# Kernel tuning notes

Measured on AMD Instinct MI355X. Metric: run time of the kernel, lower is better.

Reference implementation:

```python
import jax, jax.numpy as jnp
import numpy as np

D_MODEL = 1024
NHEAD = 16
D_HEAD = D_MODEL // NHEAD


def setup_inputs() -> dict:
    key = jax.random.key(0)
    ks = jax.random.split(key, 11)
    B, S = 4, 1024
    s = 1.0 / np.sqrt(D_MODEL)
    inp = {
        'q_in': jax.random.normal(ks[0], (B, S, D_MODEL), jnp.float32),
        'k_in': jax.random.normal(ks[1], (B, S, D_MODEL), jnp.float32),
        'v_in': jax.random.normal(ks[2], (B, S, D_MODEL), jnp.float32),
        'Wq': jax.random.normal(ks[3], (D_MODEL, D_MODEL), jnp.float32) * s,
        'bq': jnp.zeros((D_MODEL,), jnp.float32),
        'Wk': jax.random.normal(ks[4], (D_MODEL, D_MODEL), jnp.float32) * s,
        'bk': jnp.zeros((D_MODEL,), jnp.float32),
        'Wv': jax.random.normal(ks[5], (D_MODEL, D_MODEL), jnp.float32) * s,
        'bv': jnp.zeros((D_MODEL,), jnp.float32),
        'Wo': jax.random.normal(ks[6], (D_MODEL, D_MODEL), jnp.float32) * s,
        'bo': jnp.zeros((D_MODEL,), jnp.float32),
    }
    return inp


def reference(q_in, k_in, v_in, Wq, bq, Wk, bk, Wv, bv, Wo, bo):
    B, Sq, _ = q_in.shape
    Sk = k_in.shape[1]
    # Linear projections (torch Linear: x @ W.T + b; here W stored as [in, out])
    Q = q_in @ Wq + bq
    K = k_in @ Wk + bk
    V = v_in @ Wv + bv
    # [B, H, S, Dh]
    Qh = Q.reshape(B, Sq, NHEAD, D_HEAD).transpose(0, 2, 1, 3)
    Kh = K.reshape(B, Sk, NHEAD, D_HEAD).transpose(0, 2, 1, 3)
    Vh = V.reshape(B, Sk, NHEAD, D_HEAD).transpose(0, 2, 1, 3)
    scores = jnp.einsum('bhqd,bhkd->bhqk', Qh, Kh) / jnp.sqrt(jnp.float32(D_HEAD))
    attn_weights = jax.nn.softmax(scores, axis=-1)
    attn = jnp.einsum('bhqk,bhkd->bhqd', attn_weights, Vh)
    attn = attn.transpose(0, 2, 1, 3).reshape(B, Sq, D_MODEL)
    out = attn @ Wo + bo
    return out
```

## Files before the change

kernel.cpp:

```cpp
#include <hip/hip_runtime.h>
#include <hip/hip_bf16.h>
#include <cstdint>
#include <cstddef>

typedef __bf16 bf16_t;
typedef __bf16 bf16x8 __attribute__((ext_vector_type(8)));
typedef __bf16 bf16x4 __attribute__((ext_vector_type(4)));
typedef float f32x4 __attribute__((ext_vector_type(4)));

#define DM 1024
#define NHEAD 16
#define DHEAD 64

#define QSCALE 0.18033688011112042f
#define PSHIFT 4.0f
#define RS 72

__device__ __forceinline__ void gload_lds16(const void* g, void* l) {
    __builtin_amdgcn_global_load_lds(
        (const __attribute__((address_space(1))) void*)g,
        (__attribute__((address_space(3))) void*)l,
        16, 0, 0);
}

__device__ __forceinline__ uint4 cvt8(float4 lo, float4 hi) {
    union { bf16_t b[8]; uint4 u; } o;
    o.b[0] = (bf16_t)lo.x; o.b[1] = (bf16_t)lo.y; o.b[2] = (bf16_t)lo.z; o.b[3] = (bf16_t)lo.w;
    o.b[4] = (bf16_t)hi.x; o.b[5] = (bf16_t)hi.y; o.b[6] = (bf16_t)hi.z; o.b[7] = (bf16_t)hi.w;
    return o.u;
}

__global__ void prep(
    const float* __restrict__ q_in, const float* __restrict__ k_in, const float* __restrict__ v_in,
    bf16_t* __restrict__ Xq, bf16_t* __restrict__ Xk, bf16_t* __restrict__ Xv,
    const float* __restrict__ w0, const float* __restrict__ w1,
    const float* __restrict__ w2, const float* __restrict__ w3,
    bf16_t* __restrict__ t0, bf16_t* __restrict__ t1,
    bf16_t* __restrict__ t2, bf16_t* __restrict__ t3)
{
    __shared__ float tile[64][65];
    int id = blockIdx.x;
    if (id < 6144) {
        int plane = id >> 11;
        int blk = id & 2047;
        const float* x = plane == 0 ? q_in : plane == 1 ? k_in : v_in;
        bf16_t* y      = plane == 0 ? Xq   : plane == 1 ? Xk   : Xv;
        int i = (blk * 256 + threadIdx.x) * 8;
        float4 lo = *(const float4*)&x[i];
        float4 hi = *(const float4*)&x[i + 4];
        *(uint4*)&y[i] = cvt8(lo, hi);
    } else {
        int t = id - 6144;
        int zi = t >> 8;
        int blk = t & 255;
        const float* w = zi == 0 ? w0 : zi == 1 ? w1 : zi == 2 ? w2 : w3;
        bf16_t* wt     = zi == 0 ? t0 : zi == 1 ? t1 : zi == 2 ? t2 : t3;
        int bx = (blk & 15) * 64;
        int by = (blk >> 4) * 64;
        int tx = threadIdx.x & 63, ty = threadIdx.x >> 6;
        for (int j = 0; j < 64; j += 4)
            tile[ty + j][tx] = w[(size_t)(by + ty + j) * DM + bx + tx];
        __syncthreads();
        int nl = threadIdx.x >> 3;
        int kl = (threadIdx.x & 7) * 8;
        for (int j = 0; j < 64; j += 32) {
            int n = nl + j;
            union { bf16_t b[8]; uint4 u; } o;
            for (int i = 0; i < 8; i++)
                o.b[i] = (bf16_t)tile[kl + i][n];
            *(uint4*)&wt[(size_t)(bx + n) * DM + by + kl] = o.u;
        }
    }
}

template <int MODE>
__device__ __forceinline__ void gemm_body(
    const bf16_t* __restrict__ A, const bf16_t* __restrict__ Bt,
    const float* __restrict__ bias, float scale,
    float* __restrict__ Cf, bf16_t* __restrict__ Cb,
    int r0, int c0, bf16_t* AsP, bf16_t* BsP)
{
    const int K = 1024;
    int tid  = threadIdx.x;
    int wave = tid >> 6;
    int lane = tid & 63;
    int quad = lane >> 4;
    int ln   = lane & 15;
    int wr   = wave >> 1;
    int wc   = wave & 1;

    f32x4 acc[4][4];
    for (int rb = 0; rb < 4; rb++)
        for (int cb = 0; cb < 4; cb++)
            acc[rb][cb] = (f32x4){0.f, 0.f, 0.f, 0.f};

    int sr = tid >> 2;
    int sk = (tid & 3) * 8;

    const bf16_t* gA0 = &A[(size_t)(r0 + sr) * K + sk];
    const bf16_t* gA1 = gA0 + (size_t)64 * K;
    const bf16_t* gB0 = &Bt[(size_t)(c0 + sr) * K + sk];
    const bf16_t* gB1 = gB0 + (size_t)64 * K;
    char* lA = (char*)AsP + wave * 1024;
    char* lB = (char*)BsP + wave * 1024;

    gload_lds16(gA0, lA);
    gload_lds16(gA1, lA + 4096);
    gload_lds16(gB0, lB);
    gload_lds16(gB1, lB + 4096);
    __syncthreads();

    int cur = 0;
    for (int k0 = 0; k0 < K; k0 += 32) {
        int nxt = cur ^ 1;
        if (k0 + 32 < K) {
            int off = nxt * 8192;
            gload_lds16(gA0 + k0 + 32, lA + off);
            gload_lds16(gA1 + k0 + 32, lA + off + 4096);
            gload_lds16(gB0 + k0 + 32, lB + off);
            gload_lds16(gB1 + k0 + 32, lB + off + 4096);
        }
        const bf16_t* Ab = AsP + cur * 4096;
        const bf16_t* Bb = BsP + cur * 4096;

        bf16x8 af[4], bfv[4];
        for (int rb = 0; rb < 4; rb++)
            af[rb] = *(const bf16x8*)&Ab[(wr * 64 + rb * 16 + ln) * 32 + quad * 8];
        for (int cb = 0; cb < 4; cb++)
            bfv[cb] = *(const bf16x8*)&Bb[(wc * 64 + cb * 16 + ln) * 32 + quad * 8];
        for (int rb = 0; rb < 4; rb++)
            for (int cb = 0; cb < 4; cb++)
                acc[rb][cb] = __builtin_amdgcn_mfma_f32_16x16x32_bf16(af[rb], bfv[cb], acc[rb][cb], 0, 0, 0);

        __syncthreads();
        cur = nxt;
    }

    for (int rb = 0; rb < 4; rb++) {
        for (int cb = 0; cb < 4; cb++) {
            int C = c0 + wc * 64 + cb * 16 + ln;
            for (int r = 0; r < 4; r++) {
                int R = r0 + wr * 64 + rb * 16 + quad * 4 + r;
                float v = acc[rb][cb][r];
                if (MODE == 0) {
                    Cf[(size_t)R * DM + C] = v + bias[C];
                } else if (MODE == 1) {
                    int b = R >> 10, s = R & 1023;
                    int h = C >> 6,  d = C & 63;
                    Cb[(((size_t)b * NHEAD + h) * 1024 + s) * DHEAD + d] =
                        (bf16_t)((v + bias[C]) * scale);
                } else {
                    Cb[((size_t)(C >> 10) * 1024 + R) * 1024 + (C & 1023)] =
                        (bf16_t)(v + bias[R]);
                }
            }
        }
    }
}

__global__ __launch_bounds__(256) void gemm_qkv(
    const bf16_t* __restrict__ Xq, const bf16_t* __restrict__ Xk, const bf16_t* __restrict__ Xv,
    const bf16_t* __restrict__ Wtq, const bf16_t* __restrict__ Wtk, const bf16_t* __restrict__ Wtv,
    const float* __restrict__ bq, const float* __restrict__ bk, const float* __restrict__ bv,
    bf16_t* __restrict__ Qd, bf16_t* __restrict__ Kd, bf16_t* __restrict__ Vt)
{
    __shared__ __align__(16) bf16_t As[2 * 128 * 32];
    __shared__ __align__(16) bf16_t Bs[2 * 128 * 32];
    int z = blockIdx.z;
    if (z == 0) {
        gemm_body<1>(Xq, Wtq, bq, QSCALE, nullptr, Qd,
                     blockIdx.x * 128, blockIdx.y * 128, As, Bs);
    } else if (z == 1) {
        gemm_body<1>(Xk, Wtk, bk, 1.0f, nullptr, Kd,
                     blockIdx.x * 128, blockIdx.y * 128, As, Bs);
    } else {
        gemm_body<2>(Wtv, Xv, bv, 1.0f, nullptr, Vt,
                     blockIdx.y * 128, blockIdx.x * 128, As, Bs);
    }
}

__global__ __launch_bounds__(256) void gemm_out(
    const bf16_t* __restrict__ At, const bf16_t* __restrict__ Wto,
    const float* __restrict__ bo, float* __restrict__ out)
{
    const int K = 1024;
    __shared__ __align__(16) bf16_t As[2 * 64 * 32];
    __shared__ __align__(16) bf16_t Bs[2 * 128 * 32];

    int tid  = threadIdx.x;
    int wave = tid >> 6;
    int lane = tid & 63;
    int quad = lane >> 4;
    int ln   = lane & 15;

    int r0 = blockIdx.x * 64;
    int c0 = blockIdx.y * 128;

    f32x4 acc[4][2];
    for (int rb = 0; rb < 4; rb++)
        for (int cb = 0; cb < 2; cb++)
            acc[rb][cb] = (f32x4){0.f, 0.f, 0.f, 0.f};

    int sr = tid >> 2;
    int sk = (tid & 3) * 8;

    const bf16_t* gA0 = At  + (size_t)(r0 + sr) * K + sk;
    const bf16_t* gB0 = Wto + (size_t)(c0 + sr) * K + sk;
    const bf16_t* gB1 = gB0 + (size_t)64 * K;
    char* lA = (char*)As + wave * 1024;
    char* lB = (char*)Bs + wave * 1024;

    gload_lds16(gA0, lA);
    gload_lds16(gB0, lB);
    gload_lds16(gB1, lB + 4096);
    __syncthreads();

    int cur = 0;
    for (int k0 = 0; k0 < K; k0 += 32) {
        int nxt = cur ^ 1;
        if (k0 + 32 < K) {
            gload_lds16(gA0 + k0 + 32, lA + nxt * 4096);
            gload_lds16(gB0 + k0 + 32, lB + nxt * 8192);
            gload_lds16(gB1 + k0 + 32, lB + nxt * 8192 + 4096);
        }
        const bf16_t* Ab = As + cur * 2048;
        const bf16_t* Bb = Bs + cur * 4096;

        bf16x8 af[4], bfv[2];
        for (int rb = 0; rb < 4; rb++)
            af[rb] = *(const bf16x8*)&Ab[(rb * 16 + ln) * 32 + quad * 8];
        for (int cb = 0; cb < 2; cb++)
            bfv[cb] = *(const bf16x8*)&Bb[(wave * 32 + cb * 16 + ln) * 32 + quad * 8];
        for (int rb = 0; rb < 4; rb++)
            for (int cb = 0; cb < 2; cb++)
                acc[rb][cb] = __builtin_amdgcn_mfma_f32_16x16x32_bf16(af[rb], bfv[cb], acc[rb][cb], 0, 0, 0);

        __syncthreads();
        cur = nxt;
    }

    for (int rb = 0; rb < 4; rb++) {
        for (int cb = 0; cb < 2; cb++) {
            int C = c0 + wave * 32 + cb * 16 + ln;
            float bn = bo[C];
            for (int r = 0; r < 4; r++) {
                int R = r0 + rb * 16 + quad * 4 + r;
                out[(size_t)R * DM + C] = acc[rb][cb][r] + bn;
            }
        }
    }
}

__global__ __launch_bounds__(256) void attn6(
    const bf16_t* __restrict__ Q,
    const bf16_t* __restrict__ K,
    const bf16_t* __restrict__ Vt,
    bf16_t* __restrict__ O)
{
    __shared__ __align__(16) bf16_t Ks[64 * RS];
    __shared__ __align__(16) bf16_t Vs[64 * RS];
    __shared__ __align__(16) bf16_t Ps[4][32 * RS];

    int tid  = threadIdx.x;
    int wave = tid >> 6;
    int lane = tid & 63;
    int quad = lane >> 4;
    int ln   = lane & 15;

    int bh = blockIdx.x;
    int q0w = blockIdx.y * 128 + wave * 32;

    const bf16_t* Qb = Q  + (size_t)bh * 65536;
    const bf16_t* Kb = K  + (size_t)bh * 65536;
    const bf16_t* Vb = Vt + (size_t)bh * 65536;

    int srow = tid >> 3;
    int scol = (tid & 7) * 8;
    const bf16_t* gK0 = Kb + (size_t)srow * 64 + scol;
    const bf16_t* gK1 = gK0 + 32 * 64;
    const bf16_t* gV0 = Vb + (size_t)srow * 1024 + scol;
    const bf16_t* gV1 = gV0 + 32 * 1024;

    bf16x8 aq0[2], aq1[2];
    for (int h = 0; h < 2; h++) {
        aq0[h] = *(const bf16x8*)&Qb[(size_t)(q0w + h * 16 + ln) * 64 + quad * 8];
        aq1[h] = *(const bf16x8*)&Qb[(size_t)(q0w + h * 16 + ln) * 64 + 32 + quad * 8];
    }

    uint4 rK0 = *(const uint4*)gK0;
    uint4 rK1 = *(const uint4*)gK1;
    uint4 rV0 = *(const uint4*)gV0;
    uint4 rV1 = *(const uint4*)gV1;

    float l_lane[2] = {0.f, 0.f};
    f32x4 o_acc[2][4];
    for (int h = 0; h < 2; h++)
        for (int cb = 0; cb < 4; cb++)
            o_acc[h][cb] = (f32x4){0.f, 0.f, 0.f, 0.f};

    bf16_t* Pw = Ps[wave];

    for (int kt = 0; kt < 16; kt++) {
        __syncthreads();
        *(uint4*)&Ks[srow * RS + scol]        = rK0;
        *(uint4*)&Ks[(32 + srow) * RS + scol] = rK1;
        *(uint4*)&Vs[srow * RS + scol]        = rV0;
        *(uint4*)&Vs[(32 + srow) * RS + scol] = rV1;
        __syncthreads();

        if (kt < 15) {
            gK0 += 4096; gK1 += 4096; gV0 += 64; gV1 += 64;
            rK0 = *(const uint4*)gK0;
            rK1 = *(const uint4*)gK1;
            rV0 = *(const uint4*)gV0;
            rV1 = *(const uint4*)gV1;
        }

        f32x4 sc[4][2];
        for (int kb = 0; kb < 4; kb++) {
            bf16x8 kf0 = *(const bf16x8*)&Ks[(kb * 16 + ln) * RS + quad * 8];
            bf16x8 kf1 = *(const bf16x8*)&Ks[(kb * 16 + ln) * RS + 32 + quad * 8];
            for (int h = 0; h < 2; h++) {
                f32x4 a = (f32x4){0.f, 0.f, 0.f, 0.f};
                a = __builtin_amdgcn_mfma_f32_16x16x32_bf16(kf0, aq0[h], a, 0, 0, 0);
                a = __builtin_amdgcn_mfma_f32_16x16x32_bf16(kf1, aq1[h], a, 0, 0, 0);
                sc[kb][h] = a;
            }
        }

        for (int kb = 0; kb < 4; kb++) {
            for (int h = 0; h < 2; h++) {
                float p0 = __builtin_amdgcn_exp2f(sc[kb][h][0] - PSHIFT);
                float p1 = __builtin_amdgcn_exp2f(sc[kb][h][1] - PSHIFT);
                float p2 = __builtin_amdgcn_exp2f(sc[kb][h][2] - PSHIFT);
                float p3 = __builtin_amdgcn_exp2f(sc[kb][h][3] - PSHIFT);
                l_lane[h] += (p0 + p1) + (p2 + p3);
                bf16x4 pk = (bf16x4){(bf16_t)p0, (bf16_t)p1, (bf16_t)p2, (bf16_t)p3};
                *(bf16x4*)&Pw[(h * 16 + ln) * RS + kb * 16 + quad * 4] = pk;
            }
        }

        for (int kc = 0; kc < 2; kc++) {
            bf16x8 ap0 = *(const bf16x8*)&Pw[ln * RS + kc * 32 + quad * 8];
            bf16x8 ap1 = *(const bf16x8*)&Pw[(16 + ln) * RS + kc * 32 + quad * 8];
            for (int cb = 0; cb < 4; cb++) {
                bf16x8 vf = *(const bf16x8*)&Vs[(cb * 16 + ln) * RS + kc * 32 + quad * 8];
                o_acc[0][cb] = __builtin_amdgcn_mfma_f32_16x16x32_bf16(ap0, vf, o_acc[0][cb], 0, 0, 0);
                o_acc[1][cb] = __builtin_amdgcn_mfma_f32_16x16x32_bf16(ap1, vf, o_acc[1][cb], 0, 0, 0);
            }
        }
    }

    int b = bh >> 4, hd = bh & 15;
    for (int h = 0; h < 2; h++) {
        float l = l_lane[h];
        l += __shfl_xor(l, 16);
        l += __shfl_xor(l, 32);
        float invq[4];
        for (int r = 0; r < 4; r++)
            invq[r] = 1.f / __shfl(l, quad * 4 + r);
        for (int cb = 0; cb < 4; cb++) {
            for (int r = 0; r < 4; r++) {
                int q = q0w + h * 16 + quad * 4 + r;
                int d = cb * 16 + ln;
                O[((size_t)b * 1024 + q) * DM + hd * 64 + d] = (bf16_t)(o_acc[h][cb][r] * invq[r]);
            }
        }
    }
}

extern "C" void kernel_launch(void* const* d_in, const int* in_sizes, int n_in,
                              void* d_out, int out_size, void* d_ws, size_t ws_size,
                              hipStream_t stream) {
    const float* q_in = (const float*)d_in[0];
    const float* k_in = (const float*)d_in[1];
    const float* v_in = (const float*)d_in[2];
    const float* Wq   = (const float*)d_in[3];
    const float* bq   = (const float*)d_in[4];
    const float* Wk   = (const float*)d_in[5];
    const float* bk   = (const float*)d_in[6];
    const float* Wv   = (const float*)d_in[7];
    const float* bv   = (const float*)d_in[8];
    const float* Wo   = (const float*)d_in[9];
    const float* bo   = (const float*)d_in[10];

    char* ws = (char*)d_ws;
    const size_t MB = 1024ull * 1024ull;
    bf16_t* Xq  = (bf16_t*)(ws);
    bf16_t* Xk  = (bf16_t*)(ws + 8 * MB);
    bf16_t* Xv  = (bf16_t*)(ws + 16 * MB);
    bf16_t* Wtq = (bf16_t*)(ws + 24 * MB);
    bf16_t* Wtk = (bf16_t*)(ws + 26 * MB);
    bf16_t* Wtv = (bf16_t*)(ws + 28 * MB);
    bf16_t* Wto = (bf16_t*)(ws + 30 * MB);
    bf16_t* Qd  = (bf16_t*)(ws + 32 * MB);
    bf16_t* Kd  = (bf16_t*)(ws + 40 * MB);
    bf16_t* Vt  = (bf16_t*)(ws + 48 * MB);
    bf16_t* At  = Xq;

    prep<<<7168, 256, 0, stream>>>(q_in, k_in, v_in, Xq, Xk, Xv,
                                   Wq, Wk, Wv, Wo, Wtq, Wtk, Wtv, Wto);

    gemm_qkv<<<dim3(32, 8, 3), 256, 0, stream>>>(Xq, Xk, Xv,
                                                 Wtq, Wtk, Wtv, bq, bk, bv, Qd, Kd, Vt);

    attn6<<<dim3(64, 8), 256, 0, stream>>>(Qd, Kd, Vt, At);

    gemm_out<<<dim3(64, 8), 256, 0, stream>>>(At, Wto, bo, (float*)d_out);
}
```

Measured before the change: 203.7 us.

## Deepen GEMM LDS pipelining to four stages with vmcnt-based waits

Replaces the double-buffered global-to-LDS loop in the QKV and output projection GEMMs with a 4-slot ring buffer that keeps three K-tiles in flight. Each step waits with explicit s_waitcnt vmcnt counts plus a raw s_barrier, instead of a full __syncthreads drain after every tile. The aim is to hide global load latency and cut barrier stalls. In exchange, LDS use per block doubles, which may lower occupancy. Correctness now depends on the hand-set vmcnt counts and on the single barrier per step protecting the slot that gets overwritten. It also drops the unused MODE 0 output path.

```diff
diff --git a/kernel.cpp b/kernel.cpp
--- a/kernel.cpp
+++ b/kernel.cpp
@@ -15,6 +15,8 @@
 #define QSCALE 0.18033688011112042f
 #define PSHIFT 4.0f
 #define RS 72
+
+#define WAITVM(N) asm volatile("s_waitcnt vmcnt(" #N ")" ::: "memory")
 
 __device__ __forceinline__ void gload_lds16(const void* g, void* l) {
     __builtin_amdgcn_global_load_lds(
@@ -77,7 +79,7 @@
 __device__ __forceinline__ void gemm_body(
     const bf16_t* __restrict__ A, const bf16_t* __restrict__ Bt,
     const float* __restrict__ bias, float scale,
-    float* __restrict__ Cf, bf16_t* __restrict__ Cb,
+    bf16_t* __restrict__ Cb,
     int r0, int c0, bf16_t* AsP, bf16_t* BsP)
 {
     const int K = 1024;
@@ -104,25 +106,17 @@
     char* lA = (char*)AsP + wave * 1024;
     char* lB = (char*)BsP + wave * 1024;
 
-    gload_lds16(gA0, lA);
-    gload_lds16(gA1, lA + 4096);
-    gload_lds16(gB0, lB);
-    gload_lds16(gB1, lB + 4096);
-    __syncthreads();
-
-    int cur = 0;
-    for (int k0 = 0; k0 < K; k0 += 32) {
-        int nxt = cur ^ 1;
-        if (k0 + 32 < K) {
-            int off = nxt * 8192;
-            gload_lds16(gA0 + k0 + 32, lA + off);
-            gload_lds16(gA1 + k0 + 32, lA + off + 4096);
-            gload_lds16(gB0 + k0 + 32, lB + off);
-            gload_lds16(gB1 + k0 + 32, lB + off + 4096);
-        }
-        const bf16_t* Ab = AsP + cur * 4096;
-        const bf16_t* Bb = BsP + cur * 4096;
-
+    auto STAGE = [&](int s) {
+        int off = (s & 3) * 8192;
+        int k = s * 32;
+        gload_lds16(gA0 + k, lA + off);
+        gload_lds16(gA1 + k, lA + off + 4096);
+        gload_lds16(gB0 + k, lB + off);
+        gload_lds16(gB1 + k, lB + off + 4096);
+    };
+    auto COMPUTE = [&](int t) {
+        const bf16_t* Ab = AsP + (t & 3) * 4096;
+        const bf16_t* Bb = BsP + (t & 3) * 4096;
         bf16x8 af[4], bfv[4];
         for (int rb = 0; rb < 4; rb++)
             af[rb] = *(const bf16x8*)&Ab[(wr * 64 + rb * 16 + ln) * 32 + quad * 8];
@@ -131,10 +125,19 @@
         for (int rb = 0; rb < 4; rb++)
             for (int cb = 0; cb < 4; cb++)
                 acc[rb][cb] = __builtin_amdgcn_mfma_f32_16x16x32_bf16(af[rb], bfv[cb], acc[rb][cb], 0, 0, 0);
-
-        __syncthreads();
-        cur = nxt;
-    }
+    };
+
+    STAGE(0); STAGE(1); STAGE(2);
+
+    for (int t = 0; t < 29; ++t) {
+        WAITVM(8);
+        __builtin_amdgcn_s_barrier();
+        STAGE(t + 3);
+        COMPUTE(t);
+    }
+    WAITVM(8); __builtin_amdgcn_s_barrier(); COMPUTE(29);
+    WAITVM(4); __builtin_amdgcn_s_barrier(); COMPUTE(30);
+    WAITVM(0); __builtin_amdgcn_s_barrier(); COMPUTE(31);
 
     for (int rb = 0; rb < 4; rb++) {
         for (int cb = 0; cb < 4; cb++) {
@@ -142,9 +145,7 @@
             for (int r = 0; r < 4; r++) {
                 int R = r0 + wr * 64 + rb * 16 + quad * 4 + r;
                 float v = acc[rb][cb][r];
-                if (MODE == 0) {
-                    Cf[(size_t)R * DM + C] = v + bias[C];
-                } else if (MODE == 1) {
+                if (MODE == 1) {
                     int b = R >> 10, s = R & 1023;
                     int h = C >> 6,  d = C & 63;
                     Cb[(((size_t)b * NHEAD + h) * 1024 + s) * DHEAD + d] =
@@ -164,17 +165,17 @@
     const float* __restrict__ bq, const float* __restrict__ bk, const float* __restrict__ bv,
     bf16_t* __restrict__ Qd, bf16_t* __restrict__ Kd, bf16_t* __restrict__ Vt)
 {
-    __shared__ __align__(16) bf16_t As[2 * 128 * 32];
-    __shared__ __align__(16) bf16_t Bs[2 * 128 * 32];
+    __shared__ __align__(16) bf16_t As[4 * 128 * 32];
+    __shared__ __align__(16) bf16_t Bs[4 * 128 * 32];
     int z = blockIdx.z;
     if (z == 0) {
-        gemm_body<1>(Xq, Wtq, bq, QSCALE, nullptr, Qd,
+        gemm_body<1>(Xq, Wtq, bq, QSCALE, Qd,
                      blockIdx.x * 128, blockIdx.y * 128, As, Bs);
     } else if (z == 1) {
-        gemm_body<1>(Xk, Wtk, bk, 1.0f, nullptr, Kd,
+        gemm_body<1>(Xk, Wtk, bk, 1.0f, Kd,
                      blockIdx.x * 128, blockIdx.y * 128, As, Bs);
     } else {
-        gemm_body<2>(Wtv, Xv, bv, 1.0f, nullptr, Vt,
+        gemm_body<2>(Wtv, Xv, bv, 1.0f, Vt,
                      blockIdx.y * 128, blockIdx.x * 128, As, Bs);
     }
 }
@@ -184,8 +185,8 @@
     const float* __restrict__ bo, float* __restrict__ out)
 {
     const int K = 1024;
-    __shared__ __align__(16) bf16_t As[2 * 64 * 32];
-    __shared__ __align__(16) bf16_t Bs[2 * 128 * 32];
+    __shared__ __align__(16) bf16_t As[4 * 64 * 32];
+    __shared__ __align__(16) bf16_t Bs[4 * 128 * 32];
 
     int tid  = threadIdx.x;
     int wave = tid >> 6;
@@ -210,22 +211,15 @@
     char* lA = (char*)As + wave * 1024;
     char* lB = (char*)Bs + wave * 1024;
 
-    gload_lds16(gA0, lA);
-    gload_lds16(gB0, lB);
-    gload_lds16(gB1, lB + 4096);
-    __syncthreads();
-
-    int cur = 0;
-    for (int k0 = 0; k0 < K; k0 += 32) {
-        int nxt = cur ^ 1;
-        if (k0 + 32 < K) {
-            gload_lds16(gA0 + k0 + 32, lA + nxt * 4096);
-            gload_lds16(gB0 + k0 + 32, lB + nxt * 8192);
-            gload_lds16(gB1 + k0 + 32, lB + nxt * 8192 + 4096);
-        }
-        const bf16_t* Ab = As + cur * 2048;
-        const bf16_t* Bb = Bs + cur * 4096;
-
+    auto STAGE = [&](int s) {
+        int k = s * 32;
+        gload_lds16(gA0 + k, lA + (s & 3) * 4096);
+        gload_lds16(gB0 + k, lB + (s & 3) * 8192);
+        gload_lds16(gB1 + k, lB + (s & 3) * 8192 + 4096);
+    };
+    auto COMPUTE = [&](int t) {
+        const bf16_t* Ab = As + (t & 3) * 2048;
+        const bf16_t* Bb = Bs + (t & 3) * 4096;
         bf16x8 af[4], bfv[2];
         for (int rb = 0; rb < 4; rb++)
             af[rb] = *(const bf16x8*)&Ab[(rb * 16 + ln) * 32 + quad * 8];
@@ -234,10 +228,19 @@
         for (int rb = 0; rb < 4; rb++)
             for (int cb = 0; cb < 2; cb++)
                 acc[rb][cb] = __builtin_amdgcn_mfma_f32_16x16x32_bf16(af[rb], bfv[cb], acc[rb][cb], 0, 0, 0);
-
-        __syncthreads();
-        cur = nxt;
-    }
+    };
+
+    STAGE(0); STAGE(1); STAGE(2);
+
+    for (int t = 0; t < 29; ++t) {
+        WAITVM(6);
+        __builtin_amdgcn_s_barrier();
+        STAGE(t + 3);
+        COMPUTE(t);
+    }
+    WAITVM(6); __builtin_amdgcn_s_barrier(); COMPUTE(29);
+    WAITVM(3); __builtin_amdgcn_s_barrier(); COMPUTE(30);
+    WAITVM(0); __builtin_amdgcn_s_barrier(); COMPUTE(31);
 
     for (int rb = 0; rb < 4; rb++) {
         for (int cb = 0; cb < 2; cb++) {
```

Measured after the change: 216.7 us. 1.06x slower.

## Rewrite QKV GEMM with 256x256 tiles, 512 threads and triple-buffered LDS pipeline

Applied to the files above, without the earlier changes.

The QKV projection GEMM moves from 128x128 tiles with 256 threads and double buffering to 256x256 tiles with 512 threads (8 waves, each computing 128x64). Loads run two stages ahead through a three-buffer ring, using explicit vmcnt waits and raw barriers, MFMA priority raising, and a swizzled block index for L2 locality. The aim is more operand reuse per LDS load and better overlap of loads with compute. In exchange the grid shrinks to 192 blocks on a 256-CU device, register pressure rises from the 32 accumulators per lane, and LDS use grows to 96 KB per block.

```diff
diff --git a/kernel.cpp b/kernel.cpp
--- a/kernel.cpp
+++ b/kernel.cpp
@@ -15,6 +15,9 @@
 #define QSCALE 0.18033688011112042f
 #define PSHIFT 4.0f
 #define RS 72
+
+#define WAITVM(N) asm volatile("s_waitcnt vmcnt(" #N ")" ::: "memory")
+#define BARRIER() do { __builtin_amdgcn_s_barrier(); asm volatile("" ::: "memory"); } while (0)
 
 __device__ __forceinline__ void gload_lds16(const void* g, void* l) {
     __builtin_amdgcn_global_load_lds(
@@ -74,10 +77,10 @@
 }
 
 template <int MODE>
-__device__ __forceinline__ void gemm_body(
+__device__ __forceinline__ void gemm_body256(
     const bf16_t* __restrict__ A, const bf16_t* __restrict__ Bt,
     const float* __restrict__ bias, float scale,
-    float* __restrict__ Cf, bf16_t* __restrict__ Cb,
+    bf16_t* __restrict__ Cb,
     int r0, int c0, bf16_t* AsP, bf16_t* BsP)
 {
     const int K = 1024;
@@ -86,68 +89,93 @@
     int lane = tid & 63;
     int quad = lane >> 4;
     int ln   = lane & 15;
-    int wr   = wave >> 1;
-    int wc   = wave & 1;
-
-    f32x4 acc[4][4];
-    for (int rb = 0; rb < 4; rb++)
-        for (int cb = 0; cb < 4; cb++)
-            acc[rb][cb] = (f32x4){0.f, 0.f, 0.f, 0.f};
-
-    int sr = tid >> 2;
-    int sk = (tid & 3) * 8;
-
-    const bf16_t* gA0 = &A[(size_t)(r0 + sr) * K + sk];
-    const bf16_t* gA1 = gA0 + (size_t)64 * K;
-    const bf16_t* gB0 = &Bt[(size_t)(c0 + sr) * K + sk];
-    const bf16_t* gB1 = gB0 + (size_t)64 * K;
-    char* lA = (char*)AsP + wave * 1024;
-    char* lB = (char*)BsP + wave * 1024;
-
-    gload_lds16(gA0, lA);
-    gload_lds16(gA1, lA + 4096);
-    gload_lds16(gB0, lB);
-    gload_lds16(gB1, lB + 4096);
-    __syncthreads();
-
-    int cur = 0;
-    for (int k0 = 0; k0 < K; k0 += 32) {
-        int nxt = cur ^ 1;
-        if (k0 + 32 < K) {
-            int off = nxt * 8192;
-            gload_lds16(gA0 + k0 + 32, lA + off);
-            gload_lds16(gA1 + k0 + 32, lA + off + 4096);
-            gload_lds16(gB0 + k0 + 32, lB + off);
-            gload_lds16(gB1 + k0 + 32, lB + off + 4096);
-        }
-        const bf16_t* Ab = AsP + cur * 4096;
-        const bf16_t* Bb = BsP + cur * 4096;
-
-        bf16x8 af[4], bfv[4];
-        for (int rb = 0; rb < 4; rb++)
-            af[rb] = *(const bf16x8*)&Ab[(wr * 64 + rb * 16 + ln) * 32 + quad * 8];
-        for (int cb = 0; cb < 4; cb++)
-            bfv[cb] = *(const bf16x8*)&Bb[(wc * 64 + cb * 16 + ln) * 32 + quad * 8];
-        for (int rb = 0; rb < 4; rb++)
-            for (int cb = 0; cb < 4; cb++)
-                acc[rb][cb] = __builtin_amdgcn_mfma_f32_16x16x32_bf16(af[rb], bfv[cb], acc[rb][cb], 0, 0, 0);
-
-        __syncthreads();
-        cur = nxt;
-    }
-
-    for (int rb = 0; rb < 4; rb++) {
-        for (int cb = 0; cb < 4; cb++) {
-            int C = c0 + wc * 64 + cb * 16 + ln;
+    int wm   = wave >> 2;
+    int wn   = wave & 3;
+
+    f32x4 acc[8][4];
+    for (int m = 0; m < 8; m++)
+        for (int n = 0; n < 4; n++)
+            acc[m][n] = (f32x4){0.f, 0.f, 0.f, 0.f};
+
+    int srow = tid >> 2;
+    int sk   = (tid & 3) * 8;
+
+    const bf16_t* gA = &A[(size_t)(r0 + srow) * K + sk];
+    const bf16_t* gB = &Bt[(size_t)(c0 + srow) * K + sk];
+    char* lA = (char*)AsP + tid * 16;
+    char* lB = (char*)BsP + tid * 16;
+
+    auto STAGE_A = [&](int s, int b) {
+        int k = s * 32;
+        gload_lds16(gA + k, lA + b * 16384);
+        gload_lds16(gA + (size_t)128 * K + k, lA + b * 16384 + 8192);
+    };
+    auto STAGE_B = [&](int s, int b) {
+        int k = s * 32;
+        gload_lds16(gB + k, lB + b * 16384);
+        gload_lds16(gB + (size_t)128 * K + k, lB + b * 16384 + 8192);
+    };
+
+    STAGE_A(0, 0); STAGE_B(0, 0);
+    STAGE_A(1, 1); STAGE_B(1, 1);
+    WAITVM(4);
+    BARRIER();
+
+    int b = 0, b2 = 2;
+    for (int t = 0; t < 32; ++t) {
+        const bf16_t* Ab = AsP + b * 8192;
+        const bf16_t* Bb = BsP + b * 8192;
+
+        if (t < 30) STAGE_A(t + 2, b2);
+
+        bf16x8 bfr[4];
+        #pragma unroll
+        for (int nf = 0; nf < 4; nf++)
+            bfr[nf] = *(const bf16x8*)&Bb[(wn * 64 + nf * 16 + ln) * 32 + quad * 8];
+
+        bf16x8 af[4];
+        #pragma unroll
+        for (int mf = 0; mf < 4; mf++)
+            af[mf] = *(const bf16x8*)&Ab[(wm * 128 + mf * 16 + ln) * 32 + quad * 8];
+        __builtin_amdgcn_s_setprio(1);
+        #pragma unroll
+        for (int mf = 0; mf < 4; mf++)
+            #pragma unroll
+            for (int nf = 0; nf < 4; nf++)
+                acc[mf][nf] = __builtin_amdgcn_mfma_f32_16x16x32_bf16(af[mf], bfr[nf], acc[mf][nf], 0, 0, 0);
+        __builtin_amdgcn_s_setprio(0);
+
+        if (t < 30) STAGE_B(t + 2, b2);
+
+        #pragma unroll
+        for (int mf = 0; mf < 4; mf++)
+            af[mf] = *(const bf16x8*)&Ab[(wm * 128 + 64 + mf * 16 + ln) * 32 + quad * 8];
+        __builtin_amdgcn_s_setprio(1);
+        #pragma unroll
+        for (int mf = 0; mf < 4; mf++)
+            #pragma unroll
+            for (int nf = 0; nf < 4; nf++)
+                acc[4 + mf][nf] = __builtin_amdgcn_mfma_f32_16x16x32_bf16(af[mf], bfr[nf], acc[4 + mf][nf], 0, 0, 0);
+        __builtin_amdgcn_s_setprio(0);
+
+        if (t < 30)      { WAITVM(4); }
+        else if (t == 30){ WAITVM(0); }
+        if (t < 31) BARRIER();
+
+        b  = (b  == 2) ? 0 : b  + 1;
+        b2 = (b2 == 2) ? 0 : b2 + 1;
+    }
+
+    for (int m = 0; m < 8; m++) {
+        for (int nf = 0; nf < 4; nf++) {
+            int C = c0 + wn * 64 + nf * 16 + ln;
             for (int r = 0; r < 4; r++) {
-                int R = r0 + wr * 64 + rb * 16 + quad * 4 + r;
-                float v = acc[rb][cb][r];
-                if (MODE == 0) {
-                    Cf[(size_t)R * DM + C] = v + bias[C];
-                } else if (MODE == 1) {
-                    int b = R >> 10, s = R & 1023;
+                int R = r0 + wm * 128 + m * 16 + quad * 4 + r;
+                float v = acc[m][nf][r];
+                if (MODE == 1) {
+                    int bb = R >> 10, s = R & 1023;
                     int h = C >> 6,  d = C & 63;
-                    Cb[(((size_t)b * NHEAD + h) * 1024 + s) * DHEAD + d] =
+                    Cb[(((size_t)bb * NHEAD + h) * 1024 + s) * DHEAD + d] =
                         (bf16_t)((v + bias[C]) * scale);
                 } else {
                     Cb[((size_t)(C >> 10) * 1024 + R) * 1024 + (C & 1023)] =
@@ -158,24 +186,26 @@
     }
 }
 
-__global__ __launch_bounds__(256) void gemm_qkv(
+__global__ __launch_bounds__(512, 2) void gemm_qkv(
     const bf16_t* __restrict__ Xq, const bf16_t* __restrict__ Xk, const bf16_t* __restrict__ Xv,
     const bf16_t* __restrict__ Wtq, const bf16_t* __restrict__ Wtk, const bf16_t* __restrict__ Wtv,
     const float* __restrict__ bq, const float* __restrict__ bk, const float* __restrict__ bv,
     bf16_t* __restrict__ Qd, bf16_t* __restrict__ Kd, bf16_t* __restrict__ Vt)
 {
-    __shared__ __align__(16) bf16_t As[2 * 128 * 32];
-    __shared__ __align__(16) bf16_t Bs[2 * 128 * 32];
-    int z = blockIdx.z;
+    __shared__ __align__(16) bf16_t As[3 * 256 * 32];
+    __shared__ __align__(16) bf16_t Bs[3 * 256 * 32];
+    int x  = blockIdx.x;
+    int xs = (x & 7) * 8 + (x >> 3);
+    int z  = blockIdx.z;
     if (z == 0) {
-        gemm_body<1>(Xq, Wtq, bq, QSCALE, nullptr, Qd,
-                     blockIdx.x * 128, blockIdx.y * 128, As, Bs);
+        gemm_body256<1>(Xq, Wtq, bq, QSCALE, Qd,
+                        (xs >> 2) * 256, (xs & 3) * 256, As, Bs);
     } else if (z == 1) {
-        gemm_body<1>(Xk, Wtk, bk, 1.0f, nullptr, Kd,
-                     blockIdx.x * 128, blockIdx.y * 128, As, Bs);
+        gemm_body256<1>(Xk, Wtk, bk, 1.0f, Kd,
+                        (xs >> 2) * 256, (xs & 3) * 256, As, Bs);
     } else {
-        gemm_body<2>(Wtv, Xv, bv, 1.0f, nullptr, Vt,
-                     blockIdx.y * 128, blockIdx.x * 128, As, Bs);
+        gemm_body256<2>(Wtv, Xv, bv, 1.0f, Vt,
+                        (xs & 3) * 256, (xs >> 2) * 256, As, Bs);
     }
 }
 
@@ -401,7 +431,7 @@
     prep<<<7168, 256, 0, stream>>>(q_in, k_in, v_in, Xq, Xk, Xv,
                                    Wq, Wk, Wv, Wo, Wtq, Wtk, Wtv, Wto);
 
-    gemm_qkv<<<dim3(32, 8, 3), 256, 0, stream>>>(Xq, Xk, Xv,
+    gemm_qkv<<<dim3(64, 1, 3), 512, 0, stream>>>(Xq, Xk, Xv,
                                                  Wtq, Wtk, Wtv, bq, bk, bv, Qd, Kd, Vt);
 
     attn6<<<dim3(64, 8), 256, 0, stream>>>(Qd, Kd, Vt, At);
```

Measured after the change: 214.1 us. 1.05x slower.
